# Performance work log

Hardware: AMD Instinct MI355X
Metric: run time of the kernel (lower is better)

Reference implementation:

```python
import jax, jax.numpy as jnp
import numpy as np

BS, H, W = 32, 640, 640
NEG_RATIO = 3.0
POS_FRAC_THRESH = 0.95


def setup_inputs() -> dict:
    key = jax.random.key(0)
    k1, k2, k3 = jax.random.split(key, 3)
    predict = jax.random.normal(k1, (BS, 2, H, W), dtype=jnp.float32)
    vec_mask = jax.random.normal(k2, (BS, 2, H, W), dtype=jnp.float32)
    u = jax.random.uniform(k3, (BS, H, W), dtype=jnp.float32)
    # sparse positive weights (>0), exact zeros elsewhere (negatives)
    weight = jnp.where(u > POS_FRAC_THRESH, u, 0.0)
    return {"predict": predict, "vec_mask": vec_mask, "weight": weight}


def reference(predict, vec_mask, weight):
    batch_size = predict.shape[0]
    # (BS,2,H,W) -> (N,2)
    p = jnp.transpose(predict, (0, 2, 3, 1)).reshape(-1, 2)
    t = jnp.transpose(vec_mask, (0, 2, 3, 1)).reshape(-1, 2)
    w = weight.reshape(-1)  # (N,)

    pos = w > 0
    neg = w == 0
    sumPos = jnp.sum(pos)
    sumNeg = jnp.sum(neg)
    # sumhardNeg = min(3 * sumPos, sumNeg)
    sumhardNeg = jnp.minimum(NEG_RATIO * sumPos.astype(jnp.float32),
                             sumNeg.astype(jnp.float32))

    se = (p - t) ** 2  # (N,2) elementwise MSE, reduction='none'

    # positive term: sum over pos rows of se * weight (weight applied to both channels)
    posf = pos.astype(se.dtype)
    loss_pos_sum = jnp.sum(se * (w * posf)[:, None])
    weightPos_sum = 2.0 * jnp.sum(w * posf)

    # negative per-row loss, OHEM: top sumhardNeg hardest negatives
    row_neg = jnp.where(neg, se.sum(axis=1), -1.0)  # real losses >= 0
    sorted_desc = jnp.sort(row_neg)[::-1]
    rank = jnp.arange(row_neg.shape[0], dtype=jnp.float32)
    sel = rank < sumhardNeg  # k <= sumNeg, so selected entries are true neg losses
    loss_neg_sum = jnp.sum(jnp.where(sel, sorted_desc, 0.0))

    denom = weightPos_sum + sumhardNeg * 2.0
    loss = (loss_pos_sum + loss_neg_sum) / denom / batch_size
    return loss
```

## Files before the change

kernel.cpp:

```cpp
#include <hip/hip_runtime.h>

#define NROWS   13107200u
#define HW      409600u
#define N4      (NROWS/4u)
#define CBINS   4096
#define DUMMY   4095u
#define NCOPY   4
#define CSTRIDE 4097
#define TPB     256
#define BLOCKS  512
#define THREADS (BLOCKS*TPB)
#define ITERS   25

struct Ctl {
  double posLoss;
  double sumW;
};

__device__ inline float wredf(float v) {
  #pragma unroll
  for (int o = 32; o > 0; o >>= 1) v += __shfl_down(v, o, 64);
  return v;
}

__global__ __launch_bounds__(TPB)
void mainpass(const float* __restrict__ pred, const float* __restrict__ vmk,
              const float* __restrict__ wgt, Ctl* __restrict__ ctl,
              unsigned* __restrict__ ghist)
{
  __shared__ unsigned lh[NCOPY * CSTRIDE];
  for (int j = threadIdx.x; j < NCOPY * CSTRIDE; j += TPB) lh[j] = 0;
  __syncthreads();

  float posLoss = 0.f, sumW = 0.f;
  const unsigned tid = blockIdx.x * TPB + threadIdx.x;
  const unsigned copyOff = (threadIdx.x & (NCOPY - 1)) * CSTRIDE;

  #pragma unroll 1
  for (int m = 0; m < ITERS; ++m) {
    const unsigned g = tid + (unsigned)m * THREADS;
    const unsigned i = g << 2;
    const unsigned b = i / HW;
    const unsigned hw = i - b * HW;
    const size_t base = (size_t)b * (size_t)(2u * HW) + (size_t)hw;
    const float4 w4 = *(const float4*)(wgt + i);
    const float4 p0 = *(const float4*)(pred + base);
    const float4 p1 = *(const float4*)(pred + base + HW);
    const float4 t0 = *(const float4*)(vmk + base);
    const float4 t1 = *(const float4*)(vmk + base + HW);
    float se[4], wv[4];
    {
      float a, c;
      a = p0.x - t0.x; c = p1.x - t1.x; se[0] = a*a + c*c;
      a = p0.y - t0.y; c = p1.y - t1.y; se[1] = a*a + c*c;
      a = p0.z - t0.z; c = p1.z - t1.z; se[2] = a*a + c*c;
      a = p0.w - t0.w; c = p1.w - t1.w; se[3] = a*a + c*c;
    }
    wv[0] = w4.x; wv[1] = w4.y; wv[2] = w4.z; wv[3] = w4.w;
    #pragma unroll
    for (int c = 0; c < 4; ++c) {
      const float w = wv[c];
      const float s = se[c];
      posLoss = fmaf(s, w, posLoss);
      sumW += w;
      const unsigned bin = __float_as_uint(s) >> 19;
      const unsigned idx = (w == 0.f) ? bin : DUMMY;
      atomicAdd(&lh[copyOff + idx], 1u);
    }
  }

  posLoss = wredf(posLoss); sumW = wredf(sumW);
  if ((threadIdx.x & 63) == 0) {
    atomicAdd(&ctl->posLoss, (double)posLoss);
    atomicAdd(&ctl->sumW, (double)sumW);
  }
  __syncthreads();
  for (int bn = threadIdx.x; bn < CBINS; bn += TPB) {
    unsigned c = 0;
    #pragma unroll
    for (int r = 0; r < NCOPY; ++r) c += lh[r * CSTRIDE + bn];
    if (c) atomicAdd(&ghist[bn], c);
  }
}

__global__ __launch_bounds__(256)
void finish(Ctl* __restrict__ ctl, const unsigned* __restrict__ ghist,
            float* __restrict__ out)
{
  __shared__ unsigned chunkC[256];
  __shared__ double   chunkS[256];
  __shared__ unsigned binC[16];
  __shared__ double   binS[16];
  __shared__ int s_cc;
  __shared__ unsigned s_A, s_k;
  __shared__ double s_S;
  const int t = threadIdx.x;
  const unsigned posC = ghist[DUMMY];

  {
    unsigned c = 0; double s = 0.0;
    #pragma unroll
    for (int j = 0; j < CBINS / 256; ++j) {
      const unsigned bi = (unsigned)(t * (CBINS / 256) + j);
      if (bi == DUMMY) continue;
      const unsigned cnt = ghist[bi];
      if (cnt) {
        const double lo = (double)__uint_as_float(bi << 19);
        const double hi = (double)__uint_as_float((bi + 1u) << 19);
        c += cnt;
        s += (double)cnt * 0.5 * (lo + hi);
      }
    }
    chunkC[t] = c; chunkS[t] = s;
  }
  __syncthreads();
  if (t == 0) {
    const unsigned negC = NROWS - posC;
    const unsigned long long k3 = 3ull * (unsigned long long)posC;
    const unsigned k = (k3 < (unsigned long long)negC) ? (unsigned)k3 : negC;
    s_k = k;
    if (k == 0) { s_cc = -1; s_A = 0; s_S = 0.0; }
    else {
      unsigned A = 0; double S = 0.0;
      int cc = 255;
      for (; cc >= 0; --cc) {
        if (A + chunkC[cc] >= k) break;
        A += chunkC[cc]; S += chunkS[cc];
      }
      s_cc = cc; s_A = A; s_S = S;
    }
  }
  __syncthreads();
  const int cc = s_cc;
  if (cc >= 0 && t < 16) {
    const unsigned bi = (unsigned)(cc * 16 + t);
    unsigned cnt = (bi == DUMMY) ? 0u : ghist[bi];
    binC[t] = cnt;
    if (cnt) {
      const double lo = (double)__uint_as_float(bi << 19);
      const double hi = (double)__uint_as_float((bi + 1u) << 19);
      binS[t] = (double)cnt * 0.5 * (lo + hi);
    } else binS[t] = 0.0;
  }
  __syncthreads();
  if (t == 0) {
    const unsigned k = s_k;
    double sel = 0.0;
    if (k > 0) {
      unsigned A = s_A; double S = s_S;
      int j = 15;
      for (;; --j) {
        const unsigned c = binC[j];
        if (A + c >= k) {
          const unsigned need = k - A;
          const unsigned bi = (unsigned)(cc * 16 + j);
          const double lo = (double)__uint_as_float(bi << 19);
          const double hi = (double)__uint_as_float((bi + 1u) << 19);
          const double q = (double)need / (double)c;
          sel = S + (double)need * (hi - 0.5 * q * (hi - lo));
          break;
        }
        A += c; S += binS[j];
      }
    }
    const double num = ctl->posLoss + sel;
    double den = 2.0 * ctl->sumW + 2.0 * (double)k;
    if (den == 0.0) den = 1.0;
    out[0] = (float)(num / den / 32.0);
  }
}

extern "C" void kernel_launch(void* const* d_in, const int* in_sizes, int n_in,
                              void* d_out, int out_size, void* d_ws, size_t ws_size,
                              hipStream_t stream)
{
  const float* pred = (const float*)d_in[0];
  const float* vmk  = (const float*)d_in[1];
  const float* wgt  = (const float*)d_in[2];
  char* ws = (char*)d_ws;
  Ctl* ctl        = (Ctl*)ws;
  unsigned* ghist = (unsigned*)(ws + 64);
  const size_t head = 64 + CBINS * 4;

  hipMemsetAsync(d_ws, 0, head, stream);
  mainpass<<<BLOCKS, TPB, 0, stream>>>(pred, vmk, wgt, ctl, ghist);
  finish<<<1, 256, 0, stream>>>(ctl, ghist, (float*)d_out);
}
```

Baseline: 300.6 us.

## Histogram only the high-loss window of negatives with a full-range fallback pass

The main pass now builds a 512-bin histogram covering only the upper range of squared-error values. Negatives below that window are skipped, and the top bin clamps anything above it. Positives are counted directly through a warp reduction instead of a dummy histogram bin, and the grid grows to 1024 blocks. This shrinks shared memory so more blocks fit per CU, and it removes the atomics for low-loss and positive rows. If the window cannot hold the top-k negatives, or the top bin saturates, a flag triggers a fallback that re-reads the inputs and runs the original full 4096-bin histogram. That fallback adds two launches that exit early when not needed, and it doubles the memory traffic when it fires.

```diff
diff --git a/kernel.cpp b/kernel.cpp
--- a/kernel.cpp
+++ b/kernel.cpp
@@ -3,18 +3,28 @@
 #define NROWS   13107200u
 #define HW      409600u
 #define N4      (NROWS/4u)
-#define CBINS   4096
-#define DUMMY   4095u
+#define TPB     256
+#define BLOCKS  1024
+#define THREADS (BLOCKS*TPB)
+#define ITERS   13
+
+#define BIN0    2068u
+#define NBINS   512
 #define NCOPY   4
-#define CSTRIDE 4097
-#define TPB     256
-#define BLOCKS  512
-#define THREADS (BLOCKS*TPB)
-#define ITERS   25
+#define CSTRIDE 513
+
+#define FCBINS   4096
+#define FNCOPY   4
+#define FCSTRIDE 4097
+#define FBLOCKS  512
+#define FTHREADS (FBLOCKS*TPB)
+#define FITERS   25
 
 struct Ctl {
   double posLoss;
   double sumW;
+  unsigned posCnt;
+  unsigned flag;
 };
 
 __device__ inline float wredf(float v) {
@@ -22,6 +32,11 @@
   for (int o = 32; o > 0; o >>= 1) v += __shfl_down(v, o, 64);
   return v;
 }
+__device__ inline unsigned wredu(unsigned v) {
+  #pragma unroll
+  for (int o = 32; o > 0; o >>= 1) v += __shfl_down(v, o, 64);
+  return v;
+}
 
 __global__ __launch_bounds__(TPB)
 void mainpass(const float* __restrict__ pred, const float* __restrict__ vmk,
@@ -33,12 +48,14 @@
   __syncthreads();
 
   float posLoss = 0.f, sumW = 0.f;
+  unsigned posCnt = 0;
   const unsigned tid = blockIdx.x * TPB + threadIdx.x;
   const unsigned copyOff = (threadIdx.x & (NCOPY - 1)) * CSTRIDE;
 
   #pragma unroll 1
   for (int m = 0; m < ITERS; ++m) {
     const unsigned g = tid + (unsigned)m * THREADS;
+    if (g >= N4) break;
     const unsigned i = g << 2;
     const unsigned b = i / HW;
     const unsigned hw = i - b * HW;
@@ -63,19 +80,23 @@
       const float s = se[c];
       posLoss = fmaf(s, w, posLoss);
       sumW += w;
-      const unsigned bin = __float_as_uint(s) >> 19;
-      const unsigned idx = (w == 0.f) ? bin : DUMMY;
-      atomicAdd(&lh[copyOff + idx], 1u);
-    }
-  }
-
-  posLoss = wredf(posLoss); sumW = wredf(sumW);
+      posCnt += (w > 0.f) ? 1u : 0u;
+      int idx = (int)(__float_as_uint(s) >> 19) - (int)BIN0;
+      if (w == 0.f && idx >= 0) {
+        idx = idx < (int)(NBINS - 1) ? idx : (int)(NBINS - 1);
+        atomicAdd(&lh[copyOff + (unsigned)idx], 1u);
+      }
+    }
+  }
+
+  posLoss = wredf(posLoss); sumW = wredf(sumW); posCnt = wredu(posCnt);
   if ((threadIdx.x & 63) == 0) {
     atomicAdd(&ctl->posLoss, (double)posLoss);
     atomicAdd(&ctl->sumW, (double)sumW);
-  }
-  __syncthreads();
-  for (int bn = threadIdx.x; bn < CBINS; bn += TPB) {
+    atomicAdd(&ctl->posCnt, posCnt);
+  }
+  __syncthreads();
+  for (int bn = threadIdx.x; bn < NBINS; bn += TPB) {
     unsigned c = 0;
     #pragma unroll
     for (int r = 0; r < NCOPY; ++r) c += lh[r * CSTRIDE + bn];
@@ -87,6 +108,139 @@
 void finish(Ctl* __restrict__ ctl, const unsigned* __restrict__ ghist,
             float* __restrict__ out)
 {
+  __shared__ unsigned sC[256];
+  __shared__ double   sS[256];
+  __shared__ unsigned s_flag, s_k;
+  const int t = threadIdx.x;
+
+  const unsigned b0 = 2u * (unsigned)t, b1 = b0 + 1u;
+  const unsigned c0 = ghist[b0], c1 = ghist[b1];
+  double s0 = 0.0, s1 = 0.0;
+  if (c0) {
+    const double lo = (double)__uint_as_float((b0 + BIN0) << 19);
+    const double hi = (double)__uint_as_float((b0 + BIN0 + 1u) << 19);
+    s0 = (double)c0 * 0.5 * (lo + hi);
+  }
+  if (c1) {
+    const double lo = (double)__uint_as_float((b1 + BIN0) << 19);
+    const double hi = (double)__uint_as_float((b1 + BIN0 + 1u) << 19);
+    s1 = (double)c1 * 0.5 * (lo + hi);
+  }
+  sC[t] = c0 + c1; sS[t] = s0 + s1;
+  __syncthreads();
+
+  for (int off = 1; off < 256; off <<= 1) {
+    unsigned c = sC[t]; double s = sS[t];
+    if (t + off < 256) { c += sC[t + off]; s += sS[t + off]; }
+    __syncthreads();
+    sC[t] = c; sS[t] = s;
+    __syncthreads();
+  }
+
+  if (t == 0) {
+    const unsigned posC = ctl->posCnt;
+    const unsigned negC = NROWS - posC;
+    const unsigned long long k3 = 3ull * (unsigned long long)posC;
+    const unsigned k = (k3 < (unsigned long long)negC) ? (unsigned)k3 : negC;
+    s_k = k;
+    s_flag = (k > 0 && (sC[0] < k || ghist[NBINS - 1] != 0u)) ? 1u : 0u;
+    if (s_flag) ctl->flag = 1u;
+  }
+  __syncthreads();
+  if (s_flag) return;
+  const unsigned k = s_k;
+
+  if (k == 0) {
+    if (t == 0) {
+      const double num = ctl->posLoss;
+      double den = 2.0 * ctl->sumW;
+      if (den == 0.0) den = 1.0;
+      out[0] = (float)(num / den / 32.0);
+    }
+    return;
+  }
+
+  const unsigned above = (t < 255) ? sC[t + 1] : 0u;
+  if (sC[t] >= k && above < k) {
+    unsigned A = above;
+    double S = (t < 255) ? sS[t + 1] : 0.0;
+    unsigned bi, cnt;
+    if (A + c1 >= k) { bi = b1; cnt = c1; }
+    else             { A += c1; S += s1; bi = b0; cnt = c0; }
+    const unsigned need = k - A;
+    const double lo = (double)__uint_as_float((bi + BIN0) << 19);
+    const double hi = (double)__uint_as_float((bi + BIN0 + 1u) << 19);
+    const double q = (double)need / (double)cnt;
+    const double sel = S + (double)need * (hi - 0.5 * q * (hi - lo));
+    const double num = ctl->posLoss + sel;
+    double den = 2.0 * ctl->sumW + 2.0 * (double)k;
+    if (den == 0.0) den = 1.0;
+    out[0] = (float)(num / den / 32.0);
+  }
+}
+
+
+__global__ __launch_bounds__(TPB)
+void fb_main(const float* __restrict__ pred, const float* __restrict__ vmk,
+             const float* __restrict__ wgt, const Ctl* __restrict__ ctl,
+             unsigned* __restrict__ ghist2)
+{
+  __shared__ unsigned go;
+  if (threadIdx.x == 0) go = ctl->flag;
+  __syncthreads();
+  if (!go) return;
+
+  __shared__ unsigned lh[FNCOPY * FCSTRIDE];
+  for (int j = threadIdx.x; j < FNCOPY * FCSTRIDE; j += TPB) lh[j] = 0;
+  __syncthreads();
+
+  const unsigned tid = blockIdx.x * TPB + threadIdx.x;
+  const unsigned copyOff = (threadIdx.x & (FNCOPY - 1)) * FCSTRIDE;
+
+  #pragma unroll 1
+  for (int m = 0; m < FITERS; ++m) {
+    const unsigned g = tid + (unsigned)m * FTHREADS;
+    const unsigned i = g << 2;
+    const unsigned b = i / HW;
+    const unsigned hw = i - b * HW;
+    const size_t base = (size_t)b * (size_t)(2u * HW) + (size_t)hw;
+    const float4 w4 = *(const float4*)(wgt + i);
+    const float4 p0 = *(const float4*)(pred + base);
+    const float4 p1 = *(const float4*)(pred + base + HW);
+    const float4 t0 = *(const float4*)(vmk + base);
+    const float4 t1 = *(const float4*)(vmk + base + HW);
+    float se[4], wv[4];
+    {
+      float a, c;
+      a = p0.x - t0.x; c = p1.x - t1.x; se[0] = a*a + c*c;
+      a = p0.y - t0.y; c = p1.y - t1.y; se[1] = a*a + c*c;
+      a = p0.z - t0.z; c = p1.z - t1.z; se[2] = a*a + c*c;
+      a = p0.w - t0.w; c = p1.w - t1.w; se[3] = a*a + c*c;
+    }
+    wv[0] = w4.x; wv[1] = w4.y; wv[2] = w4.z; wv[3] = w4.w;
+    #pragma unroll
+    for (int c = 0; c < 4; ++c) {
+      if (wv[c] == 0.f) {
+        const unsigned bin = __float_as_uint(se[c]) >> 19;
+        atomicAdd(&lh[copyOff + bin], 1u);
+      }
+    }
+  }
+  __syncthreads();
+  for (int bn = threadIdx.x; bn < FCBINS; bn += TPB) {
+    unsigned c = 0;
+    #pragma unroll
+    for (int r = 0; r < FNCOPY; ++r) c += lh[r * FCSTRIDE + bn];
+    if (c) atomicAdd(&ghist2[bn], c);
+  }
+}
+
+__global__ __launch_bounds__(256)
+void fb_finish(const Ctl* __restrict__ ctl, const unsigned* __restrict__ ghist2,
+               float* __restrict__ out)
+{
+  if (ctl->flag == 0u) return;
+
   __shared__ unsigned chunkC[256];
   __shared__ double   chunkS[256];
   __shared__ unsigned binC[16];
@@ -95,15 +249,14 @@
   __shared__ unsigned s_A, s_k;
   __shared__ double s_S;
   const int t = threadIdx.x;
-  const unsigned posC = ghist[DUMMY];
+  const unsigned posC = ctl->posCnt;
 
   {
     unsigned c = 0; double s = 0.0;
     #pragma unroll
-    for (int j = 0; j < CBINS / 256; ++j) {
-      const unsigned bi = (unsigned)(t * (CBINS / 256) + j);
-      if (bi == DUMMY) continue;
-      const unsigned cnt = ghist[bi];
+    for (int j = 0; j < FCBINS / 256; ++j) {
+      const unsigned bi = (unsigned)(t * (FCBINS / 256) + j);
+      const unsigned cnt = ghist2[bi];
       if (cnt) {
         const double lo = (double)__uint_as_float(bi << 19);
         const double hi = (double)__uint_as_float((bi + 1u) << 19);
@@ -134,7 +287,7 @@
   const int cc = s_cc;
   if (cc >= 0 && t < 16) {
     const unsigned bi = (unsigned)(cc * 16 + t);
-    unsigned cnt = (bi == DUMMY) ? 0u : ghist[bi];
+    const unsigned cnt = ghist2[bi];
     binC[t] = cnt;
     if (cnt) {
       const double lo = (double)__uint_as_float(bi << 19);
@@ -164,7 +317,7 @@
       }
     }
     const double num = ctl->posLoss + sel;
-    double den = 2.0 * ctl->sumW + 2.0 * (double)k;
+    double den = 2.0 * ctl->sumW + 2.0 * (double)s_k;
     if (den == 0.0) den = 1.0;
     out[0] = (float)(num / den / 32.0);
   }
@@ -178,11 +331,14 @@
   const float* vmk  = (const float*)d_in[1];
   const float* wgt  = (const float*)d_in[2];
   char* ws = (char*)d_ws;
-  Ctl* ctl        = (Ctl*)ws;
-  unsigned* ghist = (unsigned*)(ws + 64);
-  const size_t head = 64 + CBINS * 4;
+  Ctl* ctl         = (Ctl*)ws;
+  unsigned* ghist  = (unsigned*)(ws + 64);
+  unsigned* ghist2 = (unsigned*)(ws + 64 + NBINS * 4);
+  const size_t head = 64 + NBINS * 4 + FCBINS * 4;
 
   hipMemsetAsync(d_ws, 0, head, stream);
   mainpass<<<BLOCKS, TPB, 0, stream>>>(pred, vmk, wgt, ctl, ghist);
   finish<<<1, 256, 0, stream>>>(ctl, ghist, (float*)d_out);
-}
+  fb_main<<<FBLOCKS, TPB, 0, stream>>>(pred, vmk, wgt, ctl, ghist2);
+  fb_finish<<<1, 256, 0, stream>>>(ctl, ghist2, (float*)d_out);
+}
```

Result: slower. 386.6 us (+28.6%).
